# Kernel tuning notes

Measured on AMD Instinct MI355X. Metric: run time of the kernel, lower is better.

Reference implementation:

```python
import jax, jax.numpy as jnp
import numpy as np

BN_EPS = 1e-5

SOBEL_X = jnp.array([[-1., 0., 1.], [-2., 0., 2.], [-1., 0., 1.]], jnp.float32).reshape(1, 1, 3, 3)
SOBEL_Y = jnp.array([[-1., -2., -1.], [0., 0., 0.], [1., 2., 1.]], jnp.float32).reshape(1, 1, 3, 3)


def _conv2d(x, w, stride, pad):
    return jax.lax.conv_general_dilated(x, w, window_strides=(stride, stride),
                                        padding=((pad, pad), (pad, pad)),
                                        dimension_numbers=('NCHW', 'OIHW', 'NCHW'))


def _resize_bilinear_align_corners(x, H, W):
    # x: [b,c,h1,w1] -> [b,c,H,W], align_corners=True
    b, c, h1, w1 = x.shape
    ys = jnp.linspace(0., h1 - 1., H)
    xs = jnp.linspace(0., w1 - 1., W)
    y0 = jnp.floor(ys).astype(jnp.int32)
    x0 = jnp.floor(xs).astype(jnp.int32)
    y1 = jnp.minimum(y0 + 1, h1 - 1)
    x1 = jnp.minimum(x0 + 1, w1 - 1)
    wy = (ys - y0)[None, None, :, None]
    wx = (xs - x0)[None, None, None, :]
    top = x[:, :, y0, :]
    bot = x[:, :, y1, :]
    top = top[:, :, :, x0] * (1. - wx) + top[:, :, :, x1] * wx
    bot = bot[:, :, :, x0] * (1. - wx) + bot[:, :, :, x1] * wx
    return top * (1. - wy) + bot * wy


def setup_inputs() -> dict:
    key = jax.random.key(0)
    ks = jax.random.split(key, 6)
    b, c, h, w = 4, 64, 128, 128
    return {
        'x': jax.random.normal(ks[0], (b, c, h, w), jnp.float32),
        'conv_w': jax.random.normal(ks[1], (c, c, 3, 3), jnp.float32) * 0.05,
        'conv_b': jax.random.normal(ks[2], (c,), jnp.float32) * 0.05,
        'bn_gamma': jnp.ones((c,), jnp.float32),
        'bn_beta': jnp.zeros((c,), jnp.float32),
        'bn_mean': jnp.zeros((c,), jnp.float32),
        'bn_var': jnp.ones((c,), jnp.float32),
        'fc1_w': jax.random.normal(ks[3], (c, c), jnp.float32) * 0.1,
        'fc2_w': jax.random.normal(ks[4], (c, c), jnp.float32) * 0.1,
        'fc3_w': jax.random.normal(ks[5], (c, c), jnp.float32) * 0.1,
    }


def reference(x, conv_w, conv_b, bn_gamma, bn_beta, bn_mean, bn_var, fc1_w, fc2_w, fc3_w):
    b, c, h, w = x.shape
    # input block: conv s2 + BN (eval) + relu
    y = _conv2d(x, conv_w, 2, 1) + conv_b[None, :, None, None]
    y = (y - bn_mean[None, :, None, None]) * jax.lax.rsqrt(bn_var + BN_EPS)[None, :, None, None]
    y = jax.nn.relu(y * bn_gamma[None, :, None, None] + bn_beta[None, :, None, None])
    b, c, h1, w1 = y.shape
    N = h1 * w1
    # pre: [b,c,h1,w1] -> [b,1,N,c]
    xp = y.reshape(b, c, N).transpose(0, 2, 1).reshape(b, 1, N, c)
    # Sobel adjacency over the N "node" axis
    sx = jnp.abs(_conv2d(xp, SOBEL_X, 1, 1)).reshape(b, N, c)
    sy = jnp.abs(_conv2d(xp, SOBEL_Y, 1, 1)).reshape(b, N, c)
    A = jnp.einsum('bnc,bmc->bnm', sx, sy)  # [b,N,N]
    # torch nn.Softmax() (no dim) on a 3D tensor => legacy dim=0 (batch axis)
    A = jax.nn.softmax(A, axis=0)
    # normalize: D^-0.5 (A + I) D^-0.5, batched
    A1 = A + jnp.eye(N, dtype=A.dtype)[None]
    dinv = A1.sum(axis=2) ** -0.5  # [b,N]
    A = dinv[:, :, None] * A1 * dinv[:, None, :]
    # GCN propagation; Conv1d k=1 no-bias == channel matmul
    xg = xp.reshape(b, N, c)
    xg = jax.nn.relu(jnp.einsum('bnm,bmc,oc->bno', A, xg, fc1_w))
    xg = jax.nn.relu(jnp.einsum('bnm,bmc,oc->bno', A, xg, fc2_w))
    xg = jnp.einsum('bnm,bmc,oc->bon', A, xg, fc3_w)  # [b,c,N]
    out = xg.reshape(b, c, h1, w1)
    return _resize_bilinear_align_corners(out, h, w)
```

## Files before the change

### kernel.cpp

```cpp
#include <hip/hip_runtime.h>
#include <hip/hip_bf16.h>

typedef float f32x4 __attribute__((ext_vector_type(4)));
typedef short bf16x8 __attribute__((ext_vector_type(8)));

#define NB 4
#define NC 64
#define NH 128
#define NW 128
#define NN 4096
#define BN_EPS_C 1e-5f

__device__ __forceinline__ void gld16(const void* g, void* l) {
    __builtin_amdgcn_global_load_lds((const __attribute__((address_space(1))) void*)g,
                                     (__attribute__((address_space(3))) void*)l, 16, 0, 0);
}
__device__ __forceinline__ unsigned pk2(float a, float b) {
    __hip_bfloat16 x = __float2bfloat16(a), y = __float2bfloat16(b);
    return (unsigned)*(unsigned short*)&x | ((unsigned)*(unsigned short*)&y << 16);
}

__global__ __launch_bounds__(256) void k_conv(
    const float* __restrict__ x, const float* __restrict__ cw, const float* __restrict__ cb,
    const float* __restrict__ bng, const float* __restrict__ bnb, const float* __restrict__ bnm,
    const float* __restrict__ bnv, float* __restrict__ xg)
{
    int b = blockIdx.y, oh = blockIdx.x;
    int tid = threadIdx.x;
    int ow = tid & 63;
    int wg = __builtin_amdgcn_readfirstlane(tid >> 6);
    float acc[16];
#pragma unroll
    for (int j = 0; j < 16; ++j) acc[j] = 0.f;
    const float* xb = x + (size_t)b * NC * NH * NW;
    int ih0 = 2 * oh - 1;
    for (int ic = 0; ic < 64; ++ic) {
        const float* xr = xb + (size_t)ic * (NH * NW);
        float v00, v01, v02, v10, v11, v12, v20, v21, v22;
        if (ih0 < 0) { v00 = v01 = v02 = 0.f; }
        else {
            const float* p = xr + ih0 * NW + 2 * ow;
            float2 t = *(const float2*)p;
            v01 = t.x; v02 = t.y;
            v00 = (ow == 0) ? 0.f : p[-1];
        }
        { const float* p = xr + (ih0 + 1) * NW + 2 * ow; float2 t = *(const float2*)p; v11 = t.x; v12 = t.y; v10 = (ow == 0) ? 0.f : p[-1]; }
        { const float* p = xr + (ih0 + 2) * NW + 2 * ow; float2 t = *(const float2*)p; v21 = t.x; v22 = t.y; v20 = (ow == 0) ? 0.f : p[-1]; }
        const float* wp = cw + ((size_t)(wg * 16) * 64 + ic) * 9;
#pragma unroll
        for (int j = 0; j < 16; ++j) {
            const float* wj = wp + (size_t)j * 576;
            acc[j] += wj[0] * v00 + wj[1] * v01 + wj[2] * v02
                    + wj[3] * v10 + wj[4] * v11 + wj[5] * v12
                    + wj[6] * v20 + wj[7] * v21 + wj[8] * v22;
        }
    }
    int n = oh * 64 + ow;
    float* outr = xg + ((size_t)b * NN + n) * 64;
#pragma unroll
    for (int j = 0; j < 16; ++j) {
        int oc = wg * 16 + j;
        float s = bng[oc] * rsqrtf(bnv[oc] + BN_EPS_C);
        float y = (acc[j] + cb[oc] - bnm[oc]) * s + bnb[oc];
        outr[oc] = fmaxf(y, 0.f);
    }
}

__global__ __launch_bounds__(256) void k_sobel(
    const float* __restrict__ xg,
    __hip_bfloat16* __restrict__ xh, __hip_bfloat16* __restrict__ xl,
    __hip_bfloat16* __restrict__ yh, __hip_bfloat16* __restrict__ yl)
{
    __shared__ float t[66][66];
    int b = blockIdx.y;
    int n0 = blockIdx.x * 64;
    int tid = threadIdx.x;
    const float* xb = xg + (size_t)b * NN * 64;
    for (int idx = tid; idx < 66 * 64; idx += 256) {
        int r = idx >> 6, c = idx & 63;
        int n = n0 - 1 + r;
        float v = (n >= 0 && n < NN) ? xb[(size_t)n * 64 + c] : 0.f;
        t[r][c + 1] = v;
    }
    for (int idx = tid; idx < 66; idx += 256) { t[idx][0] = 0.f; t[idx][65] = 0.f; }
    __syncthreads();
    int c = tid & 63, rg = tid >> 6;
    int lc = c + 1;
    for (int i = 0; i < 16; ++i) {
        int r = rg * 16 + i;
        float tm1 = t[r][lc - 1],     t0 = t[r][lc],     tp1 = t[r][lc + 1];
        float mm1 = t[r + 1][lc - 1],                    mp1 = t[r + 1][lc + 1];
        float bm1 = t[r + 2][lc - 1], b0 = t[r + 2][lc], bp1 = t[r + 2][lc + 1];
        float gx = (tp1 + 2.f * mp1 + bp1) - (tm1 + 2.f * mm1 + bm1);
        float gy = (bm1 + 2.f * b0 + bp1) - (tm1 + 2.f * t0 + tp1);
        float ax = fabsf(gx), ay = fabsf(gy);
        size_t o = ((size_t)b * NN + n0 + r) * 64 + c;
        __hip_bfloat16 h1 = __float2bfloat16(ax);
        xh[o] = h1;
        xl[o] = __float2bfloat16(ax - __bfloat162float(h1));
        __hip_bfloat16 h2 = __float2bfloat16(ay);
        yh[o] = h2;
        yl[o] = __float2bfloat16(ay - __bfloat162float(h2));
    }
}

__global__ __launch_bounds__(256, 2) void k_logits(
    const __hip_bfloat16* __restrict__ xh_, const __hip_bfloat16* __restrict__ xl_,
    const __hip_bfloat16* __restrict__ yh_, const __hip_bfloat16* __restrict__ yl_,
    __hip_bfloat16* __restrict__ A, float* __restrict__ rowsum)
{
    __shared__ __align__(16) ushort xs[2][2][4096];
    const ushort* xh = (const ushort*)xh_;
    const ushort* xl = (const ushort*)xl_;
    const ushort* yh = (const ushort*)yh_;
    const ushort* yl = (const ushort*)yl_;
    int tid = threadIdx.x, lane = tid & 63;
    int wv = __builtin_amdgcn_readfirstlane(tid >> 6);
    int l15 = lane & 15, lg = lane >> 4;
    int m0 = blockIdx.x * 128, n0 = blockIdx.y * 64;

    f32x4 acc[4][2][4];
#pragma unroll
    for (int b = 0; b < 4; ++b)
#pragma unroll
        for (int t = 0; t < 2; ++t)
#pragma unroll
            for (int u = 0; u < 4; ++u) acc[b][t][u] = (f32x4){0.f, 0.f, 0.f, 0.f};

#define STAGEX(buf, b_) do { \
    _Pragma("unroll") \
    for (int p = 0; p < 2; ++p) { \
        int ch = p * 256 + tid; \
        int r = ch >> 3; \
        int sc = ((ch & 7) ^ (r & 7)) * 8; \
        gld16(xh + ((size_t)(b_) * NN + n0 + r) * 64 + sc, (char*)xs[buf][0] + ch * 16); \
        gld16(xl + ((size_t)(b_) * NN + n0 + r) * 64 + sc, (char*)xs[buf][1] + ch * 16); \
    } \
} while (0)

#define YLOAD(Y, b_) do { \
    _Pragma("unroll") \
    for (int t = 0; t < 2; ++t) { \
        size_t rb = ((size_t)(b_) * NN + m0 + wv * 32 + t * 16 + l15) * 64 + lg * 8; \
        Y[t][0][0] = *(const bf16x8*)(yh + rb); \
        Y[t][1][0] = *(const bf16x8*)(yh + rb + 32); \
        Y[t][0][1] = *(const bf16x8*)(yl + rb); \
        Y[t][1][1] = *(const bf16x8*)(yl + rb + 32); \
    } \
} while (0)

#define COMPUTE(buf, Y, b_) do { \
    _Pragma("unroll") \
    for (int ks = 0; ks < 2; ++ks) { \
        bf16x8 xf[4][2]; \
        _Pragma("unroll") \
        for (int u = 0; u < 4; ++u) { \
            int r = u * 16 + l15; \
            int c16 = (ks * 4 + lg) ^ (r & 7); \
            xf[u][0] = *(const bf16x8*)((const char*)xs[buf][0] + r * 128 + c16 * 16); \
            xf[u][1] = *(const bf16x8*)((const char*)xs[buf][1] + r * 128 + c16 * 16); \
        } \
        _Pragma("unroll") \
        for (int t = 0; t < 2; ++t) \
            _Pragma("unroll") \
            for (int u = 0; u < 4; ++u) { \
                f32x4 a = acc[b_][t][u]; \
                a = __builtin_amdgcn_mfma_f32_16x16x32_bf16(Y[t][ks][0], xf[u][0], a, 0, 0, 0); \
                a = __builtin_amdgcn_mfma_f32_16x16x32_bf16(Y[t][ks][0], xf[u][1], a, 0, 0, 0); \
                a = __builtin_amdgcn_mfma_f32_16x16x32_bf16(Y[t][ks][1], xf[u][0], a, 0, 0, 0); \
                acc[b_][t][u] = a; \
            } \
    } \
} while (0)

    bf16x8 yA[2][2][2], yB[2][2][2];
    STAGEX(0, 0); YLOAD(yA, 0);
    __syncthreads();
    STAGEX(1, 1); YLOAD(yB, 1); COMPUTE(0, yA, 0);
    __syncthreads();
    STAGEX(0, 2); YLOAD(yA, 2); COMPUTE(1, yB, 1);
    __syncthreads();
    STAGEX(1, 3); YLOAD(yB, 3); COMPUTE(0, yA, 2);
    __syncthreads();
    COMPUTE(1, yB, 3);
#undef STAGEX
#undef YLOAD
#undef COMPUTE

    float rsum[4][4];
#pragma unroll
    for (int b = 0; b < 4; ++b)
#pragma unroll
        for (int u = 0; u < 4; ++u) rsum[b][u] = 0.f;

#pragma unroll
    for (int t = 0; t < 2; ++t)
#pragma unroll
        for (int u = 0; u < 4; ++u) {
            float av[4][4];
#pragma unroll
            for (int j = 0; j < 4; ++j) {
                float v0 = acc[0][t][u][j], v1 = acc[1][t][u][j];
                float v2 = acc[2][t][u][j], v3 = acc[3][t][u][j];
                float mx = fmaxf(fmaxf(v0, v1), fmaxf(v2, v3));
                float e0 = __expf(v0 - mx), e1 = __expf(v1 - mx);
                float e2 = __expf(v2 - mx), e3 = __expf(v3 - mx);
                float rz = 1.f / (e0 + e1 + e2 + e3);
                av[0][j] = e0 * rz; av[1][j] = e1 * rz;
                av[2][j] = e2 * rz; av[3][j] = e3 * rz;
                rsum[0][u] += av[0][j]; rsum[1][u] += av[1][j];
                rsum[2][u] += av[2][j]; rsum[3][u] += av[3][j];
            }
            int n = n0 + u * 16 + l15;
            int m = m0 + wv * 32 + t * 16 + lg * 4;
#pragma unroll
            for (int b = 0; b < 4; ++b) {
                uint2 pv;
                pv.x = pk2(av[b][0], av[b][1]);
                pv.y = pk2(av[b][2], av[b][3]);
                *(uint2*)((ushort*)A + (size_t)b * NN * NN + (size_t)n * NN + m) = pv;
            }
        }

#pragma unroll
    for (int b = 0; b < 4; ++b)
#pragma unroll
        for (int u = 0; u < 4; ++u) {
            float s = rsum[b][u];
            s += __shfl_xor(s, 16);
            s += __shfl_xor(s, 32);
            if (lane < 16)
                atomicAdd(&rowsum[(size_t)b * NN + n0 + u * 16 + l15], s);
        }
}

__global__ __launch_bounds__(256) void k_dinv(const float* __restrict__ rs, float* __restrict__ dinv)
{
    int i = blockIdx.x * 256 + threadIdx.x;
    dinv[i] = rsqrtf(rs[i] + 1.0f);
}

__global__ __launch_bounds__(256) void k_small(
    const float* __restrict__ h, const float* __restrict__ fc, const float* __restrict__ dinv,
    __hip_bfloat16* __restrict__ tT, float* __restrict__ tf)
{
    int blk = blockIdx.x;
    int b = blk >> 6, m0 = (blk & 63) * 64;
    int tid = threadIdx.x;
    int mi = tid & 63, m = m0 + mi;
    int oq = __builtin_amdgcn_readfirstlane(tid >> 6);
    const float* hr = h + ((size_t)b * NN + m) * 64;
    float hv[64];
#pragma unroll
    for (int i = 0; i < 16; ++i) {
        float4 v = *(const float4*)(hr + 4 * i);
        hv[4 * i] = v.x; hv[4 * i + 1] = v.y; hv[4 * i + 2] = v.z; hv[4 * i + 3] = v.w;
    }
    float dv = dinv[(size_t)b * NN + m];
#pragma unroll
    for (int j = 0; j < 16; ++j) {
        int o = oq * 16 + j;
        const float* wr = fc + (size_t)o * 64;
        float a = 0.f;
#pragma unroll
        for (int c2 = 0; c2 < 64; ++c2) a += hv[c2] * wr[c2];
        a *= dv;
        tf[((size_t)b * NN + m) * 64 + o] = a;
        tT[((size_t)b * 64 + o) * NN + m] = __float2bfloat16(a);
    }
}

__global__ __launch_bounds__(256) void k_big(
    const __hip_bfloat16* __restrict__ A_, const __hip_bfloat16* __restrict__ tT_,
    float* __restrict__ part)
{
    __shared__ __align__(16) ushort ab[2][4096];
    const ushort* A = (const ushort*)A_;
    const ushort* tT = (const ushort*)tT_;
    int blk = blockIdx.x;
    int ntile = blk & 63, b = (blk >> 6) & 3, ks = blk >> 8;
    int n0 = ntile * 64;
    int tid = threadIdx.x, lane = tid & 63;
    int w = __builtin_amdgcn_readfirstlane(tid >> 6);
    int l15 = lane & 15, lg = lane >> 4;
    size_t kw0 = (size_t)ks * 1024;
    const ushort* Ab = A + (size_t)b * NN * NN;
    const ushort* Tb = tT + ((size_t)b * 64 + w * 16 + l15) * NN + kw0;

    f32x4 acc[4];
#pragma unroll
    for (int ti = 0; ti < 4; ++ti) acc[ti] = (f32x4){0.f, 0.f, 0.f, 0.f};

#define STAGE(buf, s) do { \
    _Pragma("unroll") \
    for (int p = 0; p < 2; ++p) { \
        int ch = p * 256 + tid; \
        int r = ch >> 3; \
        int sc = ((ch & 7) ^ (r & 7)) * 8; \
        gld16(Ab + (size_t)(n0 + r) * NN + kw0 + (size_t)(s) * 64 + sc, (char*)ab[buf] + ch * 16); \
    } \
} while (0)

    STAGE(0, 0);
    bf16x8 bf0 = *(const bf16x8*)(Tb + lg * 8);
    bf16x8 bf1 = *(const bf16x8*)(Tb + 32 + lg * 8);
    bf16x8 nf0 = bf0, nf1 = bf1;
    __syncthreads();

    int cur = 0;
    for (int s = 0; s < 16; ++s) {
        if (s < 15) {
            STAGE(cur ^ 1, s + 1);
            nf0 = *(const bf16x8*)(Tb + (size_t)(s + 1) * 64 + lg * 8);
            nf1 = *(const bf16x8*)(Tb + (size_t)(s + 1) * 64 + 32 + lg * 8);
        }
#pragma unroll
        for (int kc = 0; kc < 2; ++kc) {
            bf16x8 bfr = (kc == 0) ? bf0 : bf1;
#pragma unroll
            for (int ti = 0; ti < 4; ++ti) {
                int r = ti * 16 + l15;
                int c16 = (kc * 4 + lg) ^ (r & 7);
                bf16x8 afr = *(const bf16x8*)((const char*)ab[cur] + r * 128 + c16 * 16);
                acc[ti] = __builtin_amdgcn_mfma_f32_16x16x32_bf16(afr, bfr, acc[ti], 0, 0, 0);
            }
        }
        bf0 = nf0; bf1 = nf1;
        __syncthreads();
        cur ^= 1;
    }
#undef STAGE

    float* pp = part + ((size_t)(ks * 4 + b) * NN + n0) * 64;
#pragma unroll
    for (int ti = 0; ti < 4; ++ti)
#pragma unroll
        for (int j = 0; j < 4; ++j)
            pp[(size_t)(ti * 16 + lg * 4 + j) * 64 + w * 16 + l15] = acc[ti][j];
}

__global__ __launch_bounds__(256) void k_red(
    const float* __restrict__ part, const float* __restrict__ tf, const float* __restrict__ dinv,
    float* __restrict__ outp, int relu)
{
    int v = blockIdx.x * 256 + threadIdx.x;
    size_t e0 = (size_t)v * 4;
    int b = (int)(e0 >> 18);
    int n = (int)((e0 >> 6) & (NN - 1));
    f32x4 u = (f32x4){0.f, 0.f, 0.f, 0.f};
#pragma unroll
    for (int s = 0; s < 4; ++s)
        u += *(const f32x4*)(part + (size_t)s * (4 * (size_t)NN * 64) + e0);
    f32x4 t = *(const f32x4*)(tf + e0);
    float dn = dinv[(size_t)b * NN + n];
    f32x4 r;
#pragma unroll
    for (int j = 0; j < 4; ++j) {
        float vv = dn * (u[j] + t[j]);
        if (relu) vv = fmaxf(vv, 0.f);
        r[j] = vv;
    }
    *(f32x4*)(outp + e0) = r;
}

__global__ __launch_bounds__(256) void k_up(const float* __restrict__ o3, float* __restrict__ outp)
{
    int b = blockIdx.y, Y = blockIdx.x;
    int tid = threadIdx.x;
    int X = tid & 127, cg = tid >> 7;
    int iy = Y * 63; int y0 = iy / 127; float wy = (float)(iy - y0 * 127) * (1.f / 127.f);
    int y1 = min(y0 + 1, 63);
    int ix = X * 63; int x0 = ix / 127; float wx = (float)(ix - x0 * 127) * (1.f / 127.f);
    int x1 = min(x0 + 1, 63);
    const float* p00 = o3 + ((size_t)b * NN + y0 * 64 + x0) * 64;
    const float* p01 = o3 + ((size_t)b * NN + y0 * 64 + x1) * 64;
    const float* p10 = o3 + ((size_t)b * NN + y1 * 64 + x0) * 64;
    const float* p11 = o3 + ((size_t)b * NN + y1 * 64 + x1) * 64;
    float w00 = (1.f - wy) * (1.f - wx), w01 = (1.f - wy) * wx;
    float w10 = wy * (1.f - wx), w11 = wy * wx;
#pragma unroll
    for (int j = 0; j < 32; ++j) {
        int ch = cg * 32 + j;
        float v = w00 * p00[ch] + w01 * p01[ch] + w10 * p10[ch] + w11 * p11[ch];
        outp[(((size_t)b * 64 + ch) * 128 + Y) * 128 + X] = v;
    }
}

extern "C" void kernel_launch(void* const* d_in, const int* in_sizes, int n_in,
                              void* d_out, int out_size, void* d_ws, size_t ws_size,
                              hipStream_t stream)
{
    const float* x   = (const float*)d_in[0];
    const float* cw  = (const float*)d_in[1];
    const float* cb  = (const float*)d_in[2];
    const float* bng = (const float*)d_in[3];
    const float* bnb = (const float*)d_in[4];
    const float* bnm = (const float*)d_in[5];
    const float* bnv = (const float*)d_in[6];
    const float* fc1 = (const float*)d_in[7];
    const float* fc2 = (const float*)d_in[8];
    const float* fc3 = (const float*)d_in[9];
    float* outp = (float*)d_out;

    char* ws = (char*)d_ws;
    size_t off = 0;
    auto alloc = [&](size_t bytes) -> void* {
        void* p = ws + off;
        off += (bytes + 255) & ~(size_t)255;
        return p;
    };
    __hip_bfloat16* Abuf = (__hip_bfloat16*)alloc((size_t)NB * NN * NN * 2);
    float* part   = (float*)alloc((size_t)4 * NB * NN * 64 * 4);
    float* xg     = (float*)alloc((size_t)NB * NN * 64 * 4);
    __hip_bfloat16* sxh = (__hip_bfloat16*)alloc((size_t)NB * NN * 64 * 2);
    __hip_bfloat16* sxl = (__hip_bfloat16*)alloc((size_t)NB * NN * 64 * 2);
    __hip_bfloat16* syh = (__hip_bfloat16*)alloc((size_t)NB * NN * 64 * 2);
    __hip_bfloat16* syl = (__hip_bfloat16*)alloc((size_t)NB * NN * 64 * 2);
    __hip_bfloat16* tT = (__hip_bfloat16*)alloc((size_t)NB * 64 * NN * 2);
    float* tf     = (float*)alloc((size_t)NB * NN * 64 * 4);
    float* h1     = (float*)alloc((size_t)NB * NN * 64 * 4);
    float* h2     = (float*)alloc((size_t)NB * NN * 64 * 4);
    float* o3     = (float*)alloc((size_t)NB * NN * 64 * 4);
    float* rowsum = (float*)alloc((size_t)NB * NN * 4);
    float* dinvb  = (float*)alloc((size_t)NB * NN * 4);

    hipMemsetAsync(rowsum, 0, (size_t)NB * NN * 4, stream);

    k_conv<<<dim3(64, 4), 256, 0, stream>>>(x, cw, cb, bng, bnb, bnm, bnv, xg);
    k_sobel<<<dim3(64, 4), 256, 0, stream>>>(xg, sxh, sxl, syh, syl);
    k_logits<<<dim3(32, 64), 256, 0, stream>>>(sxh, sxl, syh, syl, Abuf, rowsum);
    k_dinv<<<64, 256, 0, stream>>>(rowsum, dinvb);

    k_small<<<256, 256, 0, stream>>>(xg, fc1, dinvb, tT, tf);
    k_big<<<1024, 256, 0, stream>>>(Abuf, tT, part);
    k_red<<<1024, 256, 0, stream>>>(part, tf, dinvb, h1, 1);

    k_small<<<256, 256, 0, stream>>>(h1, fc2, dinvb, tT, tf);
    k_big<<<1024, 256, 0, stream>>>(Abuf, tT, part);
    k_red<<<1024, 256, 0, stream>>>(part, tf, dinvb, h2, 1);

    k_small<<<256, 256, 0, stream>>>(h2, fc3, dinvb, tT, tf);
    k_big<<<1024, 256, 0, stream>>>(Abuf, tT, part);
    k_red<<<1024, 256, 0, stream>>>(part, tf, dinvb, o3, 0);

    k_up<<<dim3(128, 4), 256, 0, stream>>>(o3, outp);
}
```

Measured before the change: 408.4 us.

## Split conv output channels across more blocks with repacked weight layout

The stride-2 conv is spread over four times as many blocks: each block now handles 16 output channels (one quad) instead of 64, with each wave computing 4 channels. A new pre-pass repacks the conv weights into a per-group contiguous layout padded to 12 floats per channel, so each wave's weights for one input channel sit together. Output is written as a single 16-byte vector store per thread. This raises occupancy on a launch that previously had only 256 blocks, at the cost of re-reading the input activations four times and adding one small kernel launch.

```diff
diff --git a/kernel.cpp b/kernel.cpp
--- a/kernel.cpp
+++ b/kernel.cpp
@@ -20,19 +20,31 @@
     return (unsigned)*(unsigned short*)&x | ((unsigned)*(unsigned short*)&y << 16);
 }
 
+__global__ __launch_bounds__(256) void k_wrep(const float* __restrict__ cw, float* __restrict__ W3)
+{
+    int idx = blockIdx.x * 256 + threadIdx.x;
+    if (idx >= 16 * 64 * 36) return;
+    int oq = idx / (64 * 36);
+    int rem = idx - oq * (64 * 36);
+    int ic = rem / 36;
+    int j = rem - ic * 36;
+    int oc4 = j / 9, kk = j - oc4 * 9;
+    W3[((size_t)oq * 64 + ic) * 48 + oc4 * 12 + kk] = cw[(((size_t)(oq * 4 + oc4)) * 64 + ic) * 9 + kk];
+}
+
 __global__ __launch_bounds__(256) void k_conv(
-    const float* __restrict__ x, const float* __restrict__ cw, const float* __restrict__ cb,
+    const float* __restrict__ x, const float* __restrict__ W3, const float* __restrict__ cb,
     const float* __restrict__ bng, const float* __restrict__ bnb, const float* __restrict__ bnm,
     const float* __restrict__ bnv, float* __restrict__ xg)
 {
-    int b = blockIdx.y, oh = blockIdx.x;
+    int oh = blockIdx.x, quad = blockIdx.y, b = blockIdx.z;
     int tid = threadIdx.x;
     int ow = tid & 63;
-    int wg = __builtin_amdgcn_readfirstlane(tid >> 6);
-    float acc[16];
-#pragma unroll
-    for (int j = 0; j < 16; ++j) acc[j] = 0.f;
+    int w = __builtin_amdgcn_readfirstlane(tid >> 6);
+    int ocg = quad * 4 + w;
+    float acc[4] = {0.f, 0.f, 0.f, 0.f};
     const float* xb = x + (size_t)b * NC * NH * NW;
+    const float* wbase = W3 + (size_t)ocg * 64 * 48;
     int ih0 = 2 * oh - 1;
     for (int ic = 0; ic < 64; ++ic) {
         const float* xr = xb + (size_t)ic * (NH * NW);
@@ -46,24 +58,26 @@
         }
         { const float* p = xr + (ih0 + 1) * NW + 2 * ow; float2 t = *(const float2*)p; v11 = t.x; v12 = t.y; v10 = (ow == 0) ? 0.f : p[-1]; }
         { const float* p = xr + (ih0 + 2) * NW + 2 * ow; float2 t = *(const float2*)p; v21 = t.x; v22 = t.y; v20 = (ow == 0) ? 0.f : p[-1]; }
-        const float* wp = cw + ((size_t)(wg * 16) * 64 + ic) * 9;
-#pragma unroll
-        for (int j = 0; j < 16; ++j) {
-            const float* wj = wp + (size_t)j * 576;
+        const float* wp = wbase + ic * 48;
+#pragma unroll
+        for (int j = 0; j < 4; ++j) {
+            const float* wj = wp + j * 12;
             acc[j] += wj[0] * v00 + wj[1] * v01 + wj[2] * v02
                     + wj[3] * v10 + wj[4] * v11 + wj[5] * v12
                     + wj[6] * v20 + wj[7] * v21 + wj[8] * v22;
         }
     }
     int n = oh * 64 + ow;
-    float* outr = xg + ((size_t)b * NN + n) * 64;
-#pragma unroll
-    for (int j = 0; j < 16; ++j) {
-        int oc = wg * 16 + j;
+    int oc0 = ocg * 4;
+    f32x4 r;
+#pragma unroll
+    for (int j = 0; j < 4; ++j) {
+        int oc = oc0 + j;
         float s = bng[oc] * rsqrtf(bnv[oc] + BN_EPS_C);
         float y = (acc[j] + cb[oc] - bnm[oc]) * s + bnb[oc];
-        outr[oc] = fmaxf(y, 0.f);
-    }
+        r[j] = fmaxf(y, 0.f);
+    }
+    *(f32x4*)(xg + ((size_t)b * NN + n) * 64 + oc0) = r;
 }
 
 __global__ __launch_bounds__(256) void k_sobel(
@@ -423,10 +437,12 @@
     float* o3     = (float*)alloc((size_t)NB * NN * 64 * 4);
     float* rowsum = (float*)alloc((size_t)NB * NN * 4);
     float* dinvb  = (float*)alloc((size_t)NB * NN * 4);
+    float* W3     = (float*)alloc((size_t)16 * 64 * 48 * 4);
 
     hipMemsetAsync(rowsum, 0, (size_t)NB * NN * 4, stream);
 
-    k_conv<<<dim3(64, 4), 256, 0, stream>>>(x, cw, cb, bng, bnb, bnm, bnv, xg);
+    k_wrep<<<144, 256, 0, stream>>>(cw, W3);
+    k_conv<<<dim3(64, 4, 4), 256, 0, stream>>>(x, W3, cb, bng, bnb, bnm, bnv, xg);
     k_sobel<<<dim3(64, 4), 256, 0, stream>>>(xg, sxh, sxl, syh, syl);
     k_logits<<<dim3(32, 64), 256, 0, stream>>>(sxh, sxl, syh, syl, Abuf, rowsum);
     k_dinv<<<64, 256, 0, stream>>>(rowsum, dinvb);
```

New measurement: 388.6 us. 4.9% less time.
